# Kernel optimization log

Hardware: AMD Instinct MI355X
Metric: run time of the kernel (lower is better)

## Reference

```python
import jax, jax.numpy as jnp
import numpy as np

N_NODES = 100000
N_EDGES = 1600000
N_GRAPHS = 256
F_IN, F_HID, F_OUT = 32, 64, 64


def setup_inputs() -> dict:
    key = jax.random.key(0)
    ks = jax.random.split(key, 9)
    x = jax.random.normal(ks[0], (N_NODES, F_IN), dtype=jnp.float32)
    edge_index = jax.random.randint(ks[1], (2, N_EDGES), 0, N_NODES, dtype=jnp.int64)
    batch = jnp.sort(jax.random.randint(ks[2], (N_NODES,), 0, N_GRAPHS, dtype=jnp.int64))
    def glorot(k, fan_in, fan_out):
        lim = (6.0 / (fan_in + fan_out)) ** 0.5
        return jax.random.uniform(k, (fan_in, fan_out), jnp.float32, -lim, lim)
    return {
        "x": x,
        "edge_index": edge_index,
        "batch": batch,
        # GraphConv layer 1: lin_rel (with bias) on aggregated msgs, lin_root (no bias) on self
        "W1_rel": glorot(ks[3], F_IN, F_HID),
        "b1_rel": jnp.zeros((F_HID,), jnp.float32),
        "W1_root": glorot(ks[4], F_IN, F_HID),
        # GraphConv layer 2
        "W2_rel": glorot(ks[5], F_HID, F_OUT),
        "b2_rel": jnp.zeros((F_OUT,), jnp.float32),
        "W2_root": glorot(ks[6], F_HID, F_OUT),
    }


def _graph_conv(h, src, dst, W_rel, b_rel, W_root):
    # PyG GraphConv (aggr='add'): out_i = W_rel @ (sum_{j->i} h_j) + b_rel + W_root @ h_i
    agg = jax.ops.segment_sum(h[src], dst, num_segments=N_NODES)  # [N, F]
    return agg @ W_rel + b_rel + h @ W_root


def reference(x, edge_index, batch, W1_rel, b1_rel, W1_root, W2_rel, b2_rel, W2_root):
    src, dst = edge_index[0], edge_index[1]
    h1 = jnp.tanh(_graph_conv(x, src, dst, W1_rel, b1_rel, W1_root))   # [N, 64]
    h2 = jnp.tanh(_graph_conv(h1, src, dst, W2_rel, b2_rel, W2_root))  # [N, 64]
    # global_mean_pool over graph ids
    sums = jax.ops.segment_sum(h2, batch, num_segments=N_GRAPHS)       # [B, 64]
    counts = jax.ops.segment_sum(jnp.ones((h2.shape[0],), h2.dtype), batch, num_segments=N_GRAPHS)
    return sums / jnp.maximum(counts, 1.0)[:, None]
```

## Files before the change

### kernel.cpp

```cpp
#include <hip/hip_runtime.h>

#define N_NODES 100000
#define N_EDGES 1600000
#define N_GRAPHS 256
#define F_IN 32
#define F_HID 64
#define F_OUT 64

#define T_WAVES 8192
#define NODES_PER_WAVE ((N_NODES + T_WAVES - 1) / T_WAVES)
#define NXCD 8
#define DPX ((N_NODES + NXCD - 1) / NXCD)

__global__ __launch_bounds__(256) void histogram_xcd(const int* __restrict__ dst,
                                                     int* __restrict__ deg) {
    int xcd = blockIdx.x & (NXCD - 1);
    int sub = blockIdx.x >> 3;
    int nsub = gridDim.x >> 3;
    int d_lo = xcd * DPX;
    int d_hi = min(d_lo + DPX, N_NODES);
    for (int e = sub * blockDim.x + threadIdx.x; e < N_EDGES; e += nsub * blockDim.x) {
        int d = __builtin_nontemporal_load(dst + e);
        if (d >= d_lo && d < d_hi) atomicAdd(&deg[d], 1);
    }
}

__global__ void scan1(const int* __restrict__ deg, int* __restrict__ end_, int* __restrict__ partials) {
    __shared__ int s[256];
    int tid = threadIdx.x;
    int i = blockIdx.x * 256 + tid;
    int v = (i < N_NODES) ? deg[i] : 0;
    s[tid] = v;
    __syncthreads();
#pragma unroll
    for (int off = 1; off < 256; off <<= 1) {
        int t = 0;
        if (tid >= off) t = s[tid - off];
        __syncthreads();
        if (tid >= off) s[tid] += t;
        __syncthreads();
    }
    if (i < N_NODES) end_[i] = s[tid];
    if (tid == 255) partials[blockIdx.x] = s[255];
}

__global__ void scan2(int* __restrict__ partials, int nb) {
    __shared__ int s[512];
    int tid = threadIdx.x;
    int v = (tid < nb) ? partials[tid] : 0;
    s[tid] = v;
    __syncthreads();
#pragma unroll
    for (int off = 1; off < 512; off <<= 1) {
        int t = 0;
        if (tid >= off) t = s[tid - off];
        __syncthreads();
        if (tid >= off) s[tid] += t;
        __syncthreads();
    }
    int excl = (tid > 0) ? s[tid - 1] : 0;
    if (tid < nb) partials[tid] = excl;
}

__global__ void scan3(const int* __restrict__ deg, int* __restrict__ end_,
                      int* __restrict__ cursor, const int* __restrict__ partials) {
    int i = blockIdx.x * 256 + threadIdx.x;
    if (i < N_NODES) {
        int e = end_[i] + partials[blockIdx.x];
        end_[i] = e;
        cursor[i] = e - deg[i];
    }
}

__global__ __launch_bounds__(256) void fill_adj_xcd(const int* __restrict__ src,
                                                    const int* __restrict__ dst,
                                                    int* __restrict__ cursor,
                                                    int* __restrict__ adj) {
    int xcd = blockIdx.x & (NXCD - 1);
    int sub = blockIdx.x >> 3;
    int nsub = gridDim.x >> 3;
    int d_lo = xcd * DPX;
    int d_hi = min(d_lo + DPX, N_NODES);
    for (int e = sub * blockDim.x + threadIdx.x; e < N_EDGES; e += nsub * blockDim.x) {
        int d = __builtin_nontemporal_load(dst + e);
        if (d >= d_lo && d < d_hi) {
            int pos = atomicAdd(&cursor[d], 1);
            adj[pos] = __builtin_nontemporal_load(src + e);
        }
    }
}

__global__ __launch_bounds__(256) void gather64_v2(const float* __restrict__ h,
        const int* __restrict__ adj, const int* __restrict__ end_, const int* __restrict__ deg,
        float* __restrict__ agg) {
    int node = (blockIdx.x * blockDim.x + threadIdx.x) >> 6;
    int lane = threadIdx.x & 63;
    if (node >= N_NODES) return;
    int e = end_[node];
    int d = deg[node];
    int s = e - d;
    int q = lane & 15;
    int r = lane >> 4;
    const float4* h4 = (const float4*)h;

    float ax = 0.f, ay = 0.f, az = 0.f, aw = 0.f;
    for (int base = 0; base < d; base += 8) {
        int i0 = base + r;
        int i1 = base + 4 + r;
        if (i0 < d) {
            int s0 = adj[s + i0];
            float4 v = h4[(size_t)s0 * 16 + q];
            ax += v.x; ay += v.y; az += v.z; aw += v.w;
        }
        if (i1 < d) {
            int s1 = adj[s + i1];
            float4 v = h4[(size_t)s1 * 16 + q];
            ax += v.x; ay += v.y; az += v.z; aw += v.w;
        }
    }
#pragma unroll
    for (int off = 16; off < 64; off <<= 1) {
        ax += __shfl_xor(ax, off);
        ay += __shfl_xor(ay, off);
        az += __shfl_xor(az, off);
        aw += __shfl_xor(aw, off);
    }
    if (r == 0) {
        float4 o; o.x = ax; o.y = ay; o.z = az; o.w = aw;
        ((float4*)agg)[(size_t)node * 16 + q] = o;
    }
}

__global__ __launch_bounds__(256) void gather32_v2(const float* __restrict__ xin,
        const int* __restrict__ adj, const int* __restrict__ end_, const int* __restrict__ deg,
        float* __restrict__ agg) {
    int node = (blockIdx.x * blockDim.x + threadIdx.x) >> 6;
    int lane = threadIdx.x & 63;
    if (node >= N_NODES) return;
    int e = end_[node];
    int d = deg[node];
    int s = e - d;
    int q = lane & 7;
    int r = lane >> 3;
    const float4* x4 = (const float4*)xin;

    float ax = 0.f, ay = 0.f, az = 0.f, aw = 0.f;
    for (int base = 0; base < d; base += 16) {
        int i0 = base + r;
        int i1 = base + 8 + r;
        if (i0 < d) {
            int s0 = adj[s + i0];
            float4 v = x4[(size_t)s0 * 8 + q];
            ax += v.x; ay += v.y; az += v.z; aw += v.w;
        }
        if (i1 < d) {
            int s1 = adj[s + i1];
            float4 v = x4[(size_t)s1 * 8 + q];
            ax += v.x; ay += v.y; az += v.z; aw += v.w;
        }
    }
#pragma unroll
    for (int off = 8; off < 64; off <<= 1) {
        ax += __shfl_xor(ax, off);
        ay += __shfl_xor(ay, off);
        az += __shfl_xor(az, off);
        aw += __shfl_xor(aw, off);
    }
    if (r == 0) {
        float4 o; o.x = ax; o.y = ay; o.z = az; o.w = aw;
        ((float4*)agg)[(size_t)node * 8 + q] = o;
    }
}

__global__ __launch_bounds__(256) void transform1_reg(const float* __restrict__ agg,
        const float* __restrict__ xin,
        const float* __restrict__ Wrel, const float* __restrict__ brel,
        const float* __restrict__ Wroot,
        float* __restrict__ h1) {
    int lane = threadIdx.x & 63;
    int wgid = __builtin_amdgcn_readfirstlane(blockIdx.x * 4 + (threadIdx.x >> 6));
    int n0 = wgid * NODES_PER_WAVE;
    if (n0 >= N_NODES) return;
    int n1 = min(n0 + NODES_PER_WAVE, N_NODES);

    float wrel[32], wroot[32];
#pragma unroll
    for (int k = 0; k < 32; ++k) {
        wrel[k] = Wrel[k * 64 + lane];
        wroot[k] = Wroot[k * 64 + lane];
    }
    float b = brel[lane];

    for (int node = n0; node < n1; ++node) {
        const float4* ar = (const float4*)(agg + (size_t)node * 32);
        const float4* xr = (const float4*)(xin + (size_t)node * 32);
        float o = b;
#pragma unroll
        for (int kk = 0; kk < 8; ++kk) {
            float4 a4 = ar[kk];
            float4 x4 = xr[kk];
            o += a4.x * wrel[kk * 4 + 0] + a4.y * wrel[kk * 4 + 1]
               + a4.z * wrel[kk * 4 + 2] + a4.w * wrel[kk * 4 + 3];
            o += x4.x * wroot[kk * 4 + 0] + x4.y * wroot[kk * 4 + 1]
               + x4.z * wroot[kk * 4 + 2] + x4.w * wroot[kk * 4 + 3];
        }
        h1[(size_t)node * 64 + lane] = tanhf(o);
    }
}

__global__ __launch_bounds__(256) void transform2_pool_reg(const float* __restrict__ agg,
        const float* __restrict__ h1,
        const float* __restrict__ Wrel, const float* __restrict__ brel,
        const float* __restrict__ Wroot,
        const int* __restrict__ batch,
        float* __restrict__ sums) {
    int lane = threadIdx.x & 63;
    int wgid = __builtin_amdgcn_readfirstlane(blockIdx.x * 4 + (threadIdx.x >> 6));
    int n0 = wgid * NODES_PER_WAVE;
    if (n0 >= N_NODES) return;
    int n1 = min(n0 + NODES_PER_WAVE, N_NODES);

    float wrel[64], wroot[64];
#pragma unroll
    for (int k = 0; k < 64; ++k) {
        wrel[k] = Wrel[k * 64 + lane];
        wroot[k] = Wroot[k * 64 + lane];
    }
    float b = brel[lane];

    float psum = 0.0f;
    int curg = batch[n0];
    for (int node = n0; node < n1; ++node) {
        const float4* ar = (const float4*)(agg + (size_t)node * 64);
        const float4* xr = (const float4*)(h1 + (size_t)node * 64);
        float o = b;
#pragma unroll
        for (int kk = 0; kk < 16; ++kk) {
            float4 a4 = ar[kk];
            float4 x4 = xr[kk];
            o += a4.x * wrel[kk * 4 + 0] + a4.y * wrel[kk * 4 + 1]
               + a4.z * wrel[kk * 4 + 2] + a4.w * wrel[kk * 4 + 3];
            o += x4.x * wroot[kk * 4 + 0] + x4.y * wroot[kk * 4 + 1]
               + x4.z * wroot[kk * 4 + 2] + x4.w * wroot[kk * 4 + 3];
        }
        float h2 = tanhf(o);
        int g = batch[node];
        if (g != curg) {
            atomicAdd(&sums[(size_t)curg * 64 + lane], psum);
            psum = 0.0f;
            curg = g;
        }
        psum += h2;
    }
    atomicAdd(&sums[(size_t)curg * 64 + lane], psum);
}

__global__ void graph_counts(const int* __restrict__ batch, float* __restrict__ counts) {
    int g = threadIdx.x;
    if (g >= N_GRAPHS) return;
    int lo = 0, hi = N_NODES;
    while (lo < hi) { int mid = (lo + hi) >> 1; if (batch[mid] < g) lo = mid + 1; else hi = mid; }
    int start = lo;
    lo = 0; hi = N_NODES;
    while (lo < hi) { int mid = (lo + hi) >> 1; if (batch[mid] <= g) lo = mid + 1; else hi = mid; }
    counts[g] = (float)(lo - start);
}

__global__ void finalize(const float* __restrict__ sums,
                         const float* __restrict__ counts,
                         float* __restrict__ out) {
    int i = blockIdx.x * blockDim.x + threadIdx.x;
    if (i < N_GRAPHS * 64) {
        float c = counts[i >> 6];
        out[i] = sums[i] / fmaxf(c, 1.0f);
    }
}

extern "C" void kernel_launch(void* const* d_in, const int* in_sizes, int n_in,
                              void* d_out, int out_size, void* d_ws, size_t ws_size,
                              hipStream_t stream) {
    const float* x       = (const float*)d_in[0];
    const int*   ei      = (const int*)d_in[1];
    const int*   batch   = (const int*)d_in[2];
    const float* W1_rel  = (const float*)d_in[3];
    const float* b1_rel  = (const float*)d_in[4];
    const float* W1_root = (const float*)d_in[5];
    const float* W2_rel  = (const float*)d_in[6];
    const float* b2_rel  = (const float*)d_in[7];
    const float* W2_root = (const float*)d_in[8];
    float* out = (float*)d_out;

    const int* src = ei;
    const int* dst = ei + N_EDGES;

    char* ws = (char*)d_ws;
    int*   deg      = (int*)(ws + 0);
    float* sums     = (float*)(ws + 400000);
    float* counts   = (float*)(ws + 465536);
    int*   end_     = (int*)(ws + 466560);
    int*   cursor   = (int*)(ws + 866560);
    int*   partials = (int*)(ws + 1266560);
    int*   adj      = (int*)(ws + 1268608);
    float* aggbuf   = (float*)(ws + 7668608);
    float* h1       = (float*)(ws + 33268608);

    hipMemsetAsync(d_ws, 0, 466560, stream);

    const int NB_NODE = (N_NODES + 255) / 256;
    histogram_xcd<<<2048, 256, 0, stream>>>(dst, deg);
    scan1<<<NB_NODE, 256, 0, stream>>>(deg, end_, partials);
    scan2<<<1, 512, 0, stream>>>(partials, NB_NODE);
    scan3<<<NB_NODE, 256, 0, stream>>>(deg, end_, cursor, partials);
    fill_adj_xcd<<<2048, 256, 0, stream>>>(src, dst, cursor, adj);

    gather32_v2<<<(N_NODES * 64 + 255) / 256, 256, 0, stream>>>(x, adj, end_, deg, aggbuf);
    transform1_reg<<<T_WAVES / 4, 256, 0, stream>>>(aggbuf, x, W1_rel, b1_rel, W1_root, h1);

    gather64_v2<<<(N_NODES * 64 + 255) / 256, 256, 0, stream>>>(h1, adj, end_, deg, aggbuf);
    transform2_pool_reg<<<T_WAVES / 4, 256, 0, stream>>>(aggbuf, h1, W2_rel, b2_rel, W2_root, batch, sums);

    graph_counts<<<1, 256, 0, stream>>>(batch, counts);
    finalize<<<(N_GRAPHS * 64 + 255) / 256, 256, 0, stream>>>(sums, counts, out);
}
```

Measured before the change: 374.9 us.

## Restructure dense transforms to 8 nodes per wave with streamed weight rows

The two dense transform kernels are rewritten so each wave handles exactly 8 consecutive nodes with 8 independent accumulators. Weight rows are loaded on the fly per k-chunk instead of being held in 64-128 registers per lane. This cuts register pressure, exposes more independent loads and FMAs per wave, and launches 12500 waves instead of 8192. In exchange each wave reloads the weights, and the pooling step makes more atomic calls because each wave covers fewer nodes. It also drops readfirstlane, and correctness relies on N_NODES being divisible by 8.

```diff
diff --git a/kernel.cpp b/kernel.cpp
--- a/kernel.cpp
+++ b/kernel.cpp
@@ -7,8 +7,7 @@
 #define F_HID 64
 #define F_OUT 64
 
-#define T_WAVES 8192
-#define NODES_PER_WAVE ((N_NODES + T_WAVES - 1) / T_WAVES)
+#define TS_BLOCKS 3125
 #define NXCD 8
 #define DPX ((N_NODES + NXCD - 1) / NXCD)
 
@@ -172,86 +171,80 @@
     }
 }
 
-__global__ __launch_bounds__(256) void transform1_reg(const float* __restrict__ agg,
+
+#define T2N(KK,N) { float4 a = A[N*16+KK]; float4 xx = X[N*16+KK]; \
+    o##N += a.x*w0 + a.y*w1 + a.z*w2 + a.w*w3 + xx.x*v0 + xx.y*v1 + xx.z*v2 + xx.w*v3; }
+
+#define T2K(KK) { \
+    float w0 = Wrel[(4*KK+0)*64+lane], w1 = Wrel[(4*KK+1)*64+lane]; \
+    float w2 = Wrel[(4*KK+2)*64+lane], w3 = Wrel[(4*KK+3)*64+lane]; \
+    float v0 = Wroot[(4*KK+0)*64+lane], v1 = Wroot[(4*KK+1)*64+lane]; \
+    float v2 = Wroot[(4*KK+2)*64+lane], v3 = Wroot[(4*KK+3)*64+lane]; \
+    T2N(KK,0) T2N(KK,1) T2N(KK,2) T2N(KK,3) T2N(KK,4) T2N(KK,5) T2N(KK,6) T2N(KK,7) }
+
+#define T1N(KK,N) { float4 a = A[N*8+KK]; float4 xx = X[N*8+KK]; \
+    o##N += a.x*w0 + a.y*w1 + a.z*w2 + a.w*w3 + xx.x*v0 + xx.y*v1 + xx.z*v2 + xx.w*v3; }
+
+#define T1K(KK) { \
+    float w0 = Wrel[(4*KK+0)*64+lane], w1 = Wrel[(4*KK+1)*64+lane]; \
+    float w2 = Wrel[(4*KK+2)*64+lane], w3 = Wrel[(4*KK+3)*64+lane]; \
+    float v0 = Wroot[(4*KK+0)*64+lane], v1 = Wroot[(4*KK+1)*64+lane]; \
+    float v2 = Wroot[(4*KK+2)*64+lane], v3 = Wroot[(4*KK+3)*64+lane]; \
+    T1N(KK,0) T1N(KK,1) T1N(KK,2) T1N(KK,3) T1N(KK,4) T1N(KK,5) T1N(KK,6) T1N(KK,7) }
+
+__global__ __launch_bounds__(256) void transform1_s(const float* __restrict__ agg,
         const float* __restrict__ xin,
         const float* __restrict__ Wrel, const float* __restrict__ brel,
         const float* __restrict__ Wroot,
         float* __restrict__ h1) {
     int lane = threadIdx.x & 63;
-    int wgid = __builtin_amdgcn_readfirstlane(blockIdx.x * 4 + (threadIdx.x >> 6));
-    int n0 = wgid * NODES_PER_WAVE;
+    int wgid = blockIdx.x * 4 + (threadIdx.x >> 6);
+    int n0 = wgid * 8;
     if (n0 >= N_NODES) return;
-    int n1 = min(n0 + NODES_PER_WAVE, N_NODES);
-
-    float wrel[32], wroot[32];
-#pragma unroll
-    for (int k = 0; k < 32; ++k) {
-        wrel[k] = Wrel[k * 64 + lane];
-        wroot[k] = Wroot[k * 64 + lane];
-    }
+    const float4* A = (const float4*)(agg + (size_t)n0 * 32);
+    const float4* X = (const float4*)(xin + (size_t)n0 * 32);
     float b = brel[lane];
-
-    for (int node = n0; node < n1; ++node) {
-        const float4* ar = (const float4*)(agg + (size_t)node * 32);
-        const float4* xr = (const float4*)(xin + (size_t)node * 32);
-        float o = b;
-#pragma unroll
-        for (int kk = 0; kk < 8; ++kk) {
-            float4 a4 = ar[kk];
-            float4 x4 = xr[kk];
-            o += a4.x * wrel[kk * 4 + 0] + a4.y * wrel[kk * 4 + 1]
-               + a4.z * wrel[kk * 4 + 2] + a4.w * wrel[kk * 4 + 3];
-            o += x4.x * wroot[kk * 4 + 0] + x4.y * wroot[kk * 4 + 1]
-               + x4.z * wroot[kk * 4 + 2] + x4.w * wroot[kk * 4 + 3];
-        }
-        h1[(size_t)node * 64 + lane] = tanhf(o);
-    }
-}
-
-__global__ __launch_bounds__(256) void transform2_pool_reg(const float* __restrict__ agg,
+    float o0 = b, o1 = b, o2 = b, o3 = b, o4 = b, o5 = b, o6 = b, o7 = b;
+
+    T1K(0) T1K(1) T1K(2) T1K(3) T1K(4) T1K(5) T1K(6) T1K(7)
+
+    float* H = h1 + (size_t)n0 * 64 + lane;
+    H[0 * 64] = tanhf(o0); H[1 * 64] = tanhf(o1);
+    H[2 * 64] = tanhf(o2); H[3 * 64] = tanhf(o3);
+    H[4 * 64] = tanhf(o4); H[5 * 64] = tanhf(o5);
+    H[6 * 64] = tanhf(o6); H[7 * 64] = tanhf(o7);
+}
+
+#define POOLSTEP(N) { \
+    if (g##N != curg) { atomicAdd(&sums[(size_t)curg * 64 + lane], psum); psum = t##N; curg = g##N; } \
+    else psum += t##N; }
+
+__global__ __launch_bounds__(256) void transform2_pool_s(const float* __restrict__ agg,
         const float* __restrict__ h1,
         const float* __restrict__ Wrel, const float* __restrict__ brel,
         const float* __restrict__ Wroot,
         const int* __restrict__ batch,
         float* __restrict__ sums) {
     int lane = threadIdx.x & 63;
-    int wgid = __builtin_amdgcn_readfirstlane(blockIdx.x * 4 + (threadIdx.x >> 6));
-    int n0 = wgid * NODES_PER_WAVE;
+    int wgid = blockIdx.x * 4 + (threadIdx.x >> 6);
+    int n0 = wgid * 8;
     if (n0 >= N_NODES) return;
-    int n1 = min(n0 + NODES_PER_WAVE, N_NODES);
-
-    float wrel[64], wroot[64];
-#pragma unroll
-    for (int k = 0; k < 64; ++k) {
-        wrel[k] = Wrel[k * 64 + lane];
-        wroot[k] = Wroot[k * 64 + lane];
-    }
+    const float4* A = (const float4*)(agg + (size_t)n0 * 64);
+    const float4* X = (const float4*)(h1 + (size_t)n0 * 64);
     float b = brel[lane];
-
-    float psum = 0.0f;
-    int curg = batch[n0];
-    for (int node = n0; node < n1; ++node) {
-        const float4* ar = (const float4*)(agg + (size_t)node * 64);
-        const float4* xr = (const float4*)(h1 + (size_t)node * 64);
-        float o = b;
-#pragma unroll
-        for (int kk = 0; kk < 16; ++kk) {
-            float4 a4 = ar[kk];
-            float4 x4 = xr[kk];
-            o += a4.x * wrel[kk * 4 + 0] + a4.y * wrel[kk * 4 + 1]
-               + a4.z * wrel[kk * 4 + 2] + a4.w * wrel[kk * 4 + 3];
-            o += x4.x * wroot[kk * 4 + 0] + x4.y * wroot[kk * 4 + 1]
-               + x4.z * wroot[kk * 4 + 2] + x4.w * wroot[kk * 4 + 3];
-        }
-        float h2 = tanhf(o);
-        int g = batch[node];
-        if (g != curg) {
-            atomicAdd(&sums[(size_t)curg * 64 + lane], psum);
-            psum = 0.0f;
-            curg = g;
-        }
-        psum += h2;
-    }
+    float o0 = b, o1 = b, o2 = b, o3 = b, o4 = b, o5 = b, o6 = b, o7 = b;
+
+    T2K(0) T2K(1) T2K(2) T2K(3) T2K(4) T2K(5) T2K(6) T2K(7)
+    T2K(8) T2K(9) T2K(10) T2K(11) T2K(12) T2K(13) T2K(14) T2K(15)
+
+    float t0 = tanhf(o0), t1 = tanhf(o1), t2 = tanhf(o2), t3 = tanhf(o3);
+    float t4 = tanhf(o4), t5 = tanhf(o5), t6 = tanhf(o6), t7 = tanhf(o7);
+    int g0 = batch[n0 + 0], g1 = batch[n0 + 1], g2 = batch[n0 + 2], g3 = batch[n0 + 3];
+    int g4 = batch[n0 + 4], g5 = batch[n0 + 5], g6 = batch[n0 + 6], g7 = batch[n0 + 7];
+
+    float psum = t0;
+    int curg = g0;
+    POOLSTEP(1) POOLSTEP(2) POOLSTEP(3) POOLSTEP(4) POOLSTEP(5) POOLSTEP(6) POOLSTEP(7)
     atomicAdd(&sums[(size_t)curg * 64 + lane], psum);
 }
 
@@ -314,10 +307,10 @@
     fill_adj_xcd<<<2048, 256, 0, stream>>>(src, dst, cursor, adj);
 
     gather32_v2<<<(N_NODES * 64 + 255) / 256, 256, 0, stream>>>(x, adj, end_, deg, aggbuf);
-    transform1_reg<<<T_WAVES / 4, 256, 0, stream>>>(aggbuf, x, W1_rel, b1_rel, W1_root, h1);
+    transform1_s<<<TS_BLOCKS, 256, 0, stream>>>(aggbuf, x, W1_rel, b1_rel, W1_root, h1);
 
     gather64_v2<<<(N_NODES * 64 + 255) / 256, 256, 0, stream>>>(h1, adj, end_, deg, aggbuf);
-    transform2_pool_reg<<<T_WAVES / 4, 256, 0, stream>>>(aggbuf, h1, W2_rel, b2_rel, W2_root, batch, sums);
+    transform2_pool_s<<<TS_BLOCKS, 256, 0, stream>>>(aggbuf, h1, W2_rel, b2_rel, W2_root, batch, sums);
 
     graph_counts<<<1, 256, 0, stream>>>(batch, counts);
     finalize<<<(N_GRAPHS * 64 + 255) / 256, 256, 0, stream>>>(sums, counts, out);
```

Result: slower. 1.329 ms (+254.6%).
